# Kernel tuning notes

Hardware: AMD Instinct MI355X
Metric: run time of the kernel (lower is better)

## Reference

```python
import jax, jax.numpy as jnp
import numpy as np
import math

FACTOR = 1

def setup_inputs() -> dict:
    key = jax.random.key(0)
    kq, kk, kv = jax.random.split(key, 3)
    B, H, L, E = 8, 8, 1024, 512
    queries = jax.random.normal(kq, (B, H, L, E), dtype=jnp.float32)
    keys = jax.random.normal(kk, (B, H, L, E), dtype=jnp.float32)
    values = jax.random.normal(kv, (B, H, L, E), dtype=jnp.float32)
    return {"queries": queries, "keys": keys, "values": values}

def _time_delay_agg_full(values, corr):
    # values: [B,H,C,Len], corr: [B,H,C,Len]  (C = seq positions, Len = feature dim here)
    length = values.shape[-1]
    top_k = int(FACTOR * math.log(length))
    weights, delay = jax.lax.top_k(corr, top_k)          # [B,H,C,k]
    tmp_corr = jax.nn.softmax(weights, axis=-1)          # [B,H,C,k]
    # gather from values.repeat(...,2) at init_index + delay  ==  circular gather mod length
    idx = (jnp.arange(length)[None, None, None, None, :] + delay[..., None]) % length  # [B,H,C,k,Len]
    gathered = jnp.take_along_axis(values[:, :, :, None, :], idx, axis=-1)             # [B,H,C,k,Len]
    return jnp.einsum('bhckl,bhck->bhcl', gathered, tmp_corr)

def reference(queries, keys, values):
    B, H, L, E = queries.shape
    S = values.shape[2]
    # L == S in this setup, so pad/slice branches are no-ops; keep slice for fidelity
    values = values[:, :, :L, :]
    keys = keys[:, :, :L, :]
    q_fft = jnp.fft.fft(queries, axis=-1)
    k_fft = jnp.fft.fft(keys, axis=-1)
    res = q_fft * jnp.conj(k_fft)
    # torch.fft.irfft(res, n=E) trims the complex input to E//2+1 before inverse; numpy/jax do the same
    corr = jnp.fft.irfft(res, n=E, axis=-1).astype(queries.dtype)  # [B,H,L,E]
    V = _time_delay_agg_full(values, corr)
    return V, jnp.transpose(corr, (0, 3, 1, 2))
```

## Files before the change

kernel.cpp:

```cpp
#include <hip/hip_runtime.h>
#include <math.h>


#define TOPK 6
#define CBAR asm volatile("" ::: "memory")

__device__ __forceinline__ float2 cmul(float2 a, float2 b) {
  return make_float2(fmaf(a.x, b.x, -(a.y * b.y)), fmaf(a.x, b.y, a.y * b.x));
}
__device__ __forceinline__ float2 cadd(float2 a, float2 b) { return make_float2(a.x + b.x, a.y + b.y); }
__device__ __forceinline__ float2 csub(float2 a, float2 b) { return make_float2(a.x - b.x, a.y - b.y); }
__device__ __forceinline__ float2 mnegi(float2 v) { return make_float2(v.y, -v.x); }

__device__ __forceinline__ unsigned bf16rne(float x) {
  unsigned t = __float_as_uint(x);
  return (t + 0x7FFFu + ((t >> 16) & 1u)) >> 16;
}

__device__ __forceinline__ unsigned wave_umax64(unsigned x) {
#define DPPMAX(ctrl)                                                          \
  {                                                                           \
    unsigned t = (unsigned)__builtin_amdgcn_update_dpp(0, (int)x, ctrl, 0xf,  \
                                                       0xf, true);            \
    x = t > x ? t : x;                                                        \
  }
  DPPMAX(0x111)
  DPPMAX(0x112)
  DPPMAX(0x114)
  DPPMAX(0x118)
  DPPMAX(0x142)
  DPPMAX(0x143)
#undef DPPMAX
  return (unsigned)__builtin_amdgcn_readlane((int)x, 63);
}

__device__ __forceinline__ void radix8(float2 y[8]) {
  float2 p0 = cadd(y[0], y[4]), p1 = csub(y[0], y[4]);
  float2 p2 = cadd(y[2], y[6]), p3 = csub(y[2], y[6]);
  float2 q0 = cadd(y[1], y[5]), q1 = csub(y[1], y[5]);
  float2 q2 = cadd(y[3], y[7]), q3 = csub(y[3], y[7]);
  float2 mp3 = mnegi(p3), mq3 = mnegi(q3);
  float2 E0 = cadd(p0, p2), E2 = csub(p0, p2);
  float2 E1 = cadd(p1, mp3), E3 = csub(p1, mp3);
  float2 O0 = cadd(q0, q2), O2 = csub(q0, q2);
  float2 O1 = cadd(q1, mq3), O3 = csub(q1, mq3);
  const float RT = 0.70710678118654752440f;
  float2 T1 = make_float2(RT * (O1.x + O1.y), RT * (O1.y - O1.x));
  float2 T2 = mnegi(O2);
  float2 T3 = make_float2(RT * (O3.y - O3.x), -RT * (O3.x + O3.y));
  y[0] = cadd(E0, O0); y[4] = csub(E0, O0);
  y[1] = cadd(E1, T1); y[5] = csub(E1, T1);
  y[2] = cadd(E2, T2); y[6] = csub(E2, T2);
  y[3] = cadd(E3, T3); y[7] = csub(E3, T3);
}

__device__ __forceinline__ void twiddle8(float2 y[8], float2 w) {
  float2 wp = w;
  y[1] = cmul(y[1], wp);
  wp = cmul(wp, w); y[2] = cmul(y[2], wp);
  wp = cmul(wp, w); y[3] = cmul(y[3], wp);
  wp = cmul(wp, w); y[4] = cmul(y[4], wp);
  wp = cmul(wp, w); y[5] = cmul(y[5], wp);
  wp = cmul(wp, w); y[6] = cmul(y[6], wp);
  wp = cmul(wp, w); y[7] = cmul(y[7], wp);
}

__device__ __forceinline__ void fft512t(float2 y[8], float* zx, float* zy,
                                        int u) {
  const int f0 = u >> 3, n0 = u & 7;
  const float N2PI = -6.28318530717958647692f;
  float s_, c_;
  radix8(y);
  __sincosf(N2PI * (float)u * (1.f / 512.f), &s_, &c_);
  twiddle8(y, make_float2(c_, s_));
#pragma unroll
  for (int r = 0; r < 8; ++r) { int s = 72 * r + u; zx[s] = y[r].x; zy[s] = y[r].y; }
  CBAR;
#pragma unroll
  for (int j = 0; j < 8; ++j) {
    int s = 72 * f0 + 8 * j + n0;
    y[j] = make_float2(zx[s], zy[s]);
  }
  radix8(y);
  __sincosf(N2PI * (float)n0 * (1.f / 64.f), &s_, &c_);
  twiddle8(y, make_float2(c_, s_));
  CBAR;
#pragma unroll
  for (int g = 0; g < 8; ++g) {
    int s = 72 * f0 + 8 * g + (n0 ^ g);
    zx[s] = y[g].x; zy[s] = y[g].y;
  }
  CBAR;
#pragma unroll
  for (int j = 0; j < 8; ++j) {
    int s = 72 * f0 + 8 * n0 + (j ^ n0);
    y[j] = make_float2(zx[s], zy[s]);
  }
  radix8(y);
}

__global__ __launch_bounds__(512, 5) void autoagg_kernel(
    const float* __restrict__ q, const float* __restrict__ kk,
    const float* __restrict__ v, float* __restrict__ outV,
    float* __restrict__ outC) {
  __shared__ float zscr[8 * 1152];
  __shared__ unsigned short tile[512 * 36];
  const int tid = threadIdx.x;
  const int u = tid & 63;
  const int w = tid >> 6;
  const int bid = blockIdx.x;
  float* zx = zscr + w * 1152;
  float* zy = zx + 576;

  const int f0 = u >> 3, n0 = u & 7;
  const int base = f0 + (n0 << 3);

#pragma unroll 1
  for (int p = 0; p < 4; ++p) {
    const int row = (bid << 5) + (p << 3) + w;
    const int rowU = __builtin_amdgcn_readfirstlane(row);
    const float* qrow = q + (size_t)rowU * 512;
    const float* krow = kk + (size_t)rowU * 512;
    const float* vrow = v + (size_t)rowU * 512;

    float2 y[8];
#pragma unroll
    for (int m = 0; m < 8; ++m)
      y[m] = make_float2(qrow[u + (m << 6)], krow[u + (m << 6)]);

    fft512t(y, zx, zy, u);

    CBAR;
#pragma unroll
    for (int r = 0; r < 8; ++r) {
      int s = 72 * r + (n0 << 3) + f0;
      zx[s] = y[r].x; zy[s] = y[r].y;
    }
    CBAR;
    const float SCL = 1.f / 2048.f;
#pragma unroll
    for (int m = 0; m < 8; ++m) {
      int fA = (m << 6) | u;
      int fB = (512 - fA) & 511;
      int sA = 72 * m + (f0 << 3) + n0;
      int sB = 72 * (fB >> 6) + (((fB >> 3) & 7) << 3) + (fB & 7);
      float Ax = zx[sA], Ay = zy[sA];
      float Bx = zx[sB], By = zy[sB];
      float sx = Ax + Bx, sy = Ay - By;
      float dx = Ax - Bx, dy = Ay + By;
      y[m] = make_float2((sx * dy - sy * dx) * SCL,
                         -fmaf(sx, dx, sy * dy) * SCL);
    }

    fft512t(y, zx, zy, u);

    const int col = (p << 3) | w;
#pragma unroll
    for (int r = 0; r < 8; ++r)
      tile[(base + (r << 6)) * 36 + col] = (unsigned short)bf16rne(y[r].x);

    unsigned key[8];
#pragma unroll
    for (int r = 0; r < 8; ++r) {
      unsigned bb = __float_as_uint(y[r].x);
      unsigned sgn = (unsigned)((int)bb >> 31);
      unsigned mono = bb ^ (sgn | 0x80000000u);
      key[r] = (mono & 0xFFFFFE00u) | (unsigned)(511 - (base + (r << 6)));
    }
    float w0 = 0.f, tw[TOPK]; int dly[TOPK];
#pragma unroll
    for (int it = 0; it < TOPK; ++it) {
      unsigned km = key[0];
#pragma unroll
      for (int i = 1; i < 8; ++i) km = key[i] > km ? key[i] : km;
      unsigned kmax = wave_umax64(km);
      unsigned mb = kmax & 0xFFFFFE00u;
      unsigned vb = (mb & 0x80000000u) ? (mb ^ 0x80000000u) : ~mb;
      float val = __uint_as_float(vb);
      if (it == 0) w0 = val;
      tw[it] = __expf(val - w0);
      dly[it] = 511 - (int)(kmax & 0x1FFu);
#pragma unroll
      for (int i = 0; i < 8; ++i) if (key[i] == kmax) key[i] = 0u;
    }
    float ssum = 0.f;
#pragma unroll
    for (int it = 0; it < TOPK; ++it) ssum += tw[it];
    const float inv = 1.f / ssum;

    float V[8] = {0.f, 0.f, 0.f, 0.f, 0.f, 0.f, 0.f, 0.f};
#pragma unroll
    for (int it = 0; it < TOPK; ++it) {
      const float twk = tw[it] * inv;
      const int d = dly[it];
#pragma unroll
      for (int i = 0; i < 8; ++i)
        V[i] = fmaf(twk, vrow[(base + (i << 6) + d) & 511], V[i]);
    }

    CBAR;
#pragma unroll
    for (int i = 0; i < 8; ++i)
      zx[76 * i + 9 * n0 + f0] = V[i];
    CBAR;
    float vt[8];
#pragma unroll
    for (int j = 0; j < 8; ++j)
      vt[j] = zx[76 * f0 + 9 * n0 + j];
    CBAR;
    float4* ov = (float4*)(outV + (size_t)rowU * 512 + (u << 3));
    ov[0] = make_float4(vt[0], vt[1], vt[2], vt[3]);
    ov[1] = make_float4(vt[4], vt[5], vt[6], vt[7]);
    CBAR;
  }

  __syncthreads();
  const int b9 = bid >> 8;
  const int h9 = (bid >> 5) & 7;
  const int l0 = (bid & 31) << 5;
#pragma unroll
  for (int round = 0; round < 8; ++round) {
    int e = (round << 6) + (tid >> 3);
    int lq = (tid & 7) << 2;
    uint2 tt = *(const uint2*)(tile + e * 36 + lq);
    float4 tv = make_float4(__uint_as_float(tt.x << 16),
                            __uint_as_float(tt.x & 0xFFFF0000u),
                            __uint_as_float(tt.y << 16),
                            __uint_as_float(tt.y & 0xFFFF0000u));
    *(float4*)(outC + (((size_t)b9 * 512 + e) * 8 + h9) * 1024 + l0 + lq) = tv;
  }
}

extern "C" void kernel_launch(void* const* d_in, const int* in_sizes, int n_in,
                              void* d_out, int out_size, void* d_ws, size_t ws_size,
                              hipStream_t stream) {
  const float* q = (const float*)d_in[0];
  const float* k = (const float*)d_in[1];
  const float* v = (const float*)d_in[2];
  float* outV = (float*)d_out;
  float* outC = (float*)d_out + (size_t)8 * 8 * 1024 * 512;
  dim3 grid(65536 / 32), block(512);
  hipLaunchKernelGGL(autoagg_kernel, grid, block, 0, stream, q, k, v, outV, outC);
}
```

Baseline: 233.0 us.

## Prefetch next row's q/k, drop LDS transpose for outV, pad tile stride

```diff
diff --git a/kernel.cpp b/kernel.cpp
--- a/kernel.cpp
+++ b/kernel.cpp
@@ -76,10 +76,14 @@
 #pragma unroll
   for (int r = 0; r < 8; ++r) { int s = 72 * r + u; zx[s] = y[r].x; zy[s] = y[r].y; }
   CBAR;
-#pragma unroll
-  for (int j = 0; j < 8; ++j) {
-    int s = 72 * f0 + 8 * j + n0;
-    y[j] = make_float2(zx[s], zy[s]);
+  {
+    const int ro[8] = {0, 4, 2, 6, 1, 5, 3, 7};
+#pragma unroll
+    for (int jj = 0; jj < 8; ++jj) {
+      int j = ro[jj];
+      int s = 72 * f0 + 8 * j + n0;
+      y[j] = make_float2(zx[s], zy[s]);
+    }
   }
   radix8(y);
   __sincosf(N2PI * (float)n0 * (1.f / 64.f), &s_, &c_);
@@ -91,20 +95,24 @@
     zx[s] = y[g].x; zy[s] = y[g].y;
   }
   CBAR;
-#pragma unroll
-  for (int j = 0; j < 8; ++j) {
-    int s = 72 * f0 + 8 * n0 + (j ^ n0);
-    y[j] = make_float2(zx[s], zy[s]);
+  {
+    const int ro[8] = {0, 4, 2, 6, 1, 5, 3, 7};
+#pragma unroll
+    for (int jj = 0; jj < 8; ++jj) {
+      int j = ro[jj];
+      int s = 72 * f0 + 8 * n0 + (j ^ n0);
+      y[j] = make_float2(zx[s], zy[s]);
+    }
   }
   radix8(y);
 }
 
-__global__ __launch_bounds__(512, 5) void autoagg_kernel(
+__global__ __launch_bounds__(512, 4) void autoagg_kernel(
     const float* __restrict__ q, const float* __restrict__ kk,
     const float* __restrict__ v, float* __restrict__ outV,
     float* __restrict__ outC) {
   __shared__ float zscr[8 * 1152];
-  __shared__ unsigned short tile[512 * 36];
+  __shared__ unsigned short tile[512 * 38];
   const int tid = threadIdx.x;
   const int u = tid & 63;
   const int w = tid >> 6;
@@ -115,18 +123,20 @@
   const int f0 = u >> 3, n0 = u & 7;
   const int base = f0 + (n0 << 3);
 
+  float2 y[8];
+  {
+    const int r0 = __builtin_amdgcn_readfirstlane((bid << 5) + w);
+    const float* qrow = q + (size_t)r0 * 512;
+    const float* krow = kk + (size_t)r0 * 512;
+#pragma unroll
+    for (int m = 0; m < 8; ++m)
+      y[m] = make_float2(qrow[u + (m << 6)], krow[u + (m << 6)]);
+  }
+
 #pragma unroll 1
   for (int p = 0; p < 4; ++p) {
-    const int row = (bid << 5) + (p << 3) + w;
-    const int rowU = __builtin_amdgcn_readfirstlane(row);
-    const float* qrow = q + (size_t)rowU * 512;
-    const float* krow = kk + (size_t)rowU * 512;
+    const int rowU = __builtin_amdgcn_readfirstlane((bid << 5) + (p << 3) + w);
     const float* vrow = v + (size_t)rowU * 512;
-
-    float2 y[8];
-#pragma unroll
-    for (int m = 0; m < 8; ++m)
-      y[m] = make_float2(qrow[u + (m << 6)], krow[u + (m << 6)]);
 
     fft512t(y, zx, zy, u);
 
@@ -157,7 +167,7 @@
     const int col = (p << 3) | w;
 #pragma unroll
     for (int r = 0; r < 8; ++r)
-      tile[(base + (r << 6)) * 36 + col] = (unsigned short)bf16rne(y[r].x);
+      tile[(base + (r << 6)) * 38 + col] = (unsigned short)bf16rne(y[r].x);
 
     unsigned key[8];
 #pragma unroll
@@ -167,6 +177,14 @@
       unsigned mono = bb ^ (sgn | 0x80000000u);
       key[r] = (mono & 0xFFFFFE00u) | (unsigned)(511 - (base + (r << 6)));
     }
+    if (p < 3) {
+      const float* qn = q + (size_t)(rowU + 8) * 512;
+      const float* kn = kk + (size_t)(rowU + 8) * 512;
+#pragma unroll
+      for (int m = 0; m < 8; ++m)
+        y[m] = make_float2(qn[u + (m << 6)], kn[u + (m << 6)]);
+    }
+
     float w0 = 0.f, tw[TOPK]; int dly[TOPK];
 #pragma unroll
     for (int it = 0; it < TOPK; ++it) {
@@ -198,19 +216,9 @@
         V[i] = fmaf(twk, vrow[(base + (i << 6) + d) & 511], V[i]);
     }
 
-    CBAR;
-#pragma unroll
-    for (int i = 0; i < 8; ++i)
-      zx[76 * i + 9 * n0 + f0] = V[i];
-    CBAR;
-    float vt[8];
-#pragma unroll
-    for (int j = 0; j < 8; ++j)
-      vt[j] = zx[76 * f0 + 9 * n0 + j];
-    CBAR;
-    float4* ov = (float4*)(outV + (size_t)rowU * 512 + (u << 3));
-    ov[0] = make_float4(vt[0], vt[1], vt[2], vt[3]);
-    ov[1] = make_float4(vt[4], vt[5], vt[6], vt[7]);
+    float* ovr = outV + (size_t)rowU * 512;
+#pragma unroll
+    for (int i = 0; i < 8; ++i) ovr[base + (i << 6)] = V[i];
     CBAR;
   }
 
@@ -222,11 +230,13 @@
   for (int round = 0; round < 8; ++round) {
     int e = (round << 6) + (tid >> 3);
     int lq = (tid & 7) << 2;
-    uint2 tt = *(const uint2*)(tile + e * 36 + lq);
-    float4 tv = make_float4(__uint_as_float(tt.x << 16),
-                            __uint_as_float(tt.x & 0xFFFF0000u),
-                            __uint_as_float(tt.y << 16),
-                            __uint_as_float(tt.y & 0xFFFF0000u));
+    const unsigned short* tr = tile + e * 38 + lq;
+    unsigned t0 = *(const unsigned*)(tr);
+    unsigned t1 = *(const unsigned*)(tr + 2);
+    float4 tv = make_float4(__uint_as_float(t0 << 16),
+                            __uint_as_float(t0 & 0xFFFF0000u),
+                            __uint_as_float(t1 << 16),
+                            __uint_as_float(t1 & 0xFFFF0000u));
     *(float4*)(outC + (((size_t)b9 * 512 + e) * 8 + h9) * 1024 + l0 + lq) = tv;
   }
 }
```

Result: slower. 282.2 us (+21.1%).
